# Kernel tuning notes

Hardware: AMD Instinct MI355X
Metric: run time of the kernel (lower is better)

The kernel has to match this reference:

```python
import jax, jax.numpy as jnp
import numpy as np

DIM = 1024
HEADS = 32
HEAD_DIM = DIM // HEADS
SR_RATIO = 2
N_RATIO = SR_RATIO * SR_RATIO  # AvgPool1d kernel/stride
BN_EPS = 1e-6


def setup_inputs() -> dict:
    key = jax.random.key(0)
    ks = jax.random.split(key, 10)
    B, N, C = 4, 2048, DIM
    s = C ** -0.5
    return {
        "x": jax.random.normal(ks[0], (B, N, C), dtype=jnp.float32),
        # torch.nn.Linear weights, shape [out, in]; applied as x @ W.T
        "Wq": jax.random.normal(ks[1], (C, C), dtype=jnp.float32) * s,
        "Wk": jax.random.normal(ks[2], (C, C), dtype=jnp.float32) * s,
        "Wv": jax.random.normal(ks[3], (C, C), dtype=jnp.float32) * s,
        "Wp": jax.random.normal(ks[4], (C, C), dtype=jnp.float32) * s,
        "bp": jax.random.normal(ks[5], (C,), dtype=jnp.float32) * 0.01,
        # BatchNorm1d (eval mode) affine + running stats over channel dim C
        "bn_gamma": jnp.ones((C,), dtype=jnp.float32),
        "bn_beta": jnp.zeros((C,), dtype=jnp.float32),
        "bn_mean": jax.random.normal(ks[6], (C,), dtype=jnp.float32) * 0.01,
        "bn_var": jnp.ones((C,), dtype=jnp.float32) + jax.random.uniform(ks[7], (C,), dtype=jnp.float32) * 0.1,
    }


def reference(x, Wq, Wk, Wv, Wp, bp, bn_gamma, bn_beta, bn_mean, bn_var):
    B, N, C = x.shape
    scale = HEAD_DIM ** -0.5
    # Q from full-resolution tokens
    q = (x @ Wq.T).reshape(B, N, HEADS, HEAD_DIM).transpose(0, 2, 1, 3)  # [B,H,N,d]
    # spatial reduction: AvgPool1d(kernel=N_RATIO, stride=N_RATIO) over tokens
    xr = x.reshape(B, N // N_RATIO, N_RATIO, C).mean(axis=2)  # [B,M,C]
    # BatchNorm1d eval: normalize channel dim with running stats
    xr = (xr - bn_mean) * jax.lax.rsqrt(bn_var + BN_EPS) * bn_gamma + bn_beta
    M = xr.shape[1]
    k = (xr @ Wk.T).reshape(B, M, HEADS, HEAD_DIM).transpose(0, 2, 1, 3)  # [B,H,M,d]
    v = (xr @ Wv.T).reshape(B, M, HEADS, HEAD_DIM).transpose(0, 2, 1, 3)  # [B,H,M,d]
    # NOTE: no softmax in the original module — raw scaled scores feed the second matmul
    attn = jnp.einsum("bhnd,bhmd->bhnm", q, k) * scale  # [B,H,N,M]
    out = jnp.einsum("bhnm,bhmd->bhnd", attn, v)        # [B,H,N,d]
    out = out.transpose(0, 2, 1, 3).reshape(B, N, C)
    return out @ Wp.T + bp
```

## Files before the change

### kernel.cpp

```cpp
#include <hip/hip_runtime.h>
#include <stdint.h>

#define DEVFN __device__ __forceinline__

typedef __attribute__((ext_vector_type(8))) short s16x8;
typedef __attribute__((ext_vector_type(4))) float f32x4;

DEVFN float bf2f(uint16_t u) {
  union { uint32_t i; float f; } v; v.i = ((uint32_t)u) << 16; return v.f;
}
DEVFN uint16_t f2bf(float f) {
  union { float f; uint32_t i; } v; v.f = f;
  uint32_t u = v.i;
  return (uint16_t)((u + 0x7FFFu + ((u >> 16) & 1u)) >> 16);
}

DEVFN void gload_lds16(const void* g, void* l) {
  __builtin_amdgcn_global_load_lds(
      (const __attribute__((address_space(1))) uint32_t*)g,
      (__attribute__((address_space(3))) uint32_t*)l, 16, 0, 0);
}

__global__ __launch_bounds__(256)
void prep_kernel(const float* __restrict__ x,
                 const float* __restrict__ bn_g, const float* __restrict__ bn_b,
                 const float* __restrict__ bn_m, const float* __restrict__ bn_v,
                 const float* __restrict__ Wk, const float* __restrict__ Wv,
                 const float* __restrict__ Wp,
                 uint16_t* __restrict__ Xh,
                 uint16_t* __restrict__ XRh,
                 uint16_t* __restrict__ Wkvh,
                 uint16_t* __restrict__ Wph)
{
  const int t = threadIdx.x;
  const int bid = blockIdx.x;
  if (bid < 2048) {
    const int prow = bid;
    const int c0 = t * 4;
    const size_t xbase = (size_t)prow * 4096 + c0;
    float s[4] = {0.f, 0.f, 0.f, 0.f};
#pragma unroll
    for (int r = 0; r < 4; ++r) {
      const float4 w = *(const float4*)(x + xbase + (size_t)r * 1024);
      const float vv[4] = { w.x, w.y, w.z, w.w };
      uint64_t wh = 0;
#pragma unroll
      for (int j = 0; j < 4; ++j) {
        wh |= ((uint64_t)f2bf(vv[j])) << (16 * j);
        s[j] += vv[j];
      }
      *(uint64_t*)(Xh + xbase + (size_t)r * 1024) = wh;
    }
    uint64_t wh = 0;
#pragma unroll
    for (int j = 0; j < 4; ++j) {
      const int c = c0 + j;
      const float y = (s[j] * 0.25f - bn_m[c]) / sqrtf(bn_v[c] + 1e-6f) * bn_g[c] + bn_b[c];
      wh |= ((uint64_t)f2bf(y)) << (16 * j);
    }
    *(uint64_t*)(XRh + (size_t)prow * 1024 + c0) = wh;
  } else {
    const int wb = bid - 2048;
    const int which = wb >> 10;
    const int i = (wb & 1023) * 256 + t;
    const float* src = (which == 0) ? Wk : (which == 1) ? Wv : Wp;
    const float4 v = ((const float4*)src)[i];
    const float vv[4] = { v.x, v.y, v.z, v.w };
    uint64_t wh = 0;
#pragma unroll
    for (int j = 0; j < 4; ++j)
      wh |= ((uint64_t)f2bf(vv[j])) << (16 * j);
    if (which == 2) {
      ((uint64_t*)Wph)[i] = wh;
    } else {
      ((uint64_t*)Wkvh)[(size_t)which * (1024 * 1024 / 4) + i] = wh;
    }
  }
}

template<int APARTS, int BPARTS, bool BATCHB, bool AMODA, int EPI, bool KSPLIT2,
         bool SMALLM>
__global__ __launch_bounds__(256, 2)
void gemm_nt(const uint16_t* __restrict__ A0, const uint16_t* __restrict__ A1,
             const uint16_t* __restrict__ B0, const uint16_t* __restrict__ B1,
             float* __restrict__ C32, uint16_t* __restrict__ Cb0,
             const float* __restrict__ bias,
             int M, int N, int K, int rows_per_batch)
{
  constexpr int BM = SMALLM ? 64 : 128, BN = 128, BK = 64;
  constexpr int WCN = SMALLM ? 4 : 2;
  constexpr int WNW = BN / WCN;
  constexpr int NREP = WNW / 16;
  constexpr int APASS = SMALLM ? 2 : 4;
  __shared__ uint16_t sA[APARTS][BM * BK];
  __shared__ uint16_t sB[BPARTS][BN * BK];

  const int t = threadIdx.x;
  const int lane = t & 63;
  const int wave = t >> 6;
  const int wr = wave / WCN, wc = wave % WCN;
  const int fq = lane >> 4, fr = lane & 15;

  const int nwg = gridDim.x;
  const int cpx = nwg >> 3;
  const int orig = blockIdx.x;
  const int swz = (orig & 7) * cpx + (orig >> 3);
  const int nbx = N >> 7;
  const int bm = (swz / nbx) * BM;
  const int bn = (swz % nbx) * BN;

  const uint16_t* Ap[2] = { A0, A1 };
  const uint16_t* Bp[2] = { B0, B1 };
  if (BATCHB) {
    const size_t boff = (size_t)(bm / rows_per_batch) * (size_t)N * (size_t)K;
    Bp[0] += boff;
    if (BPARTS > 1) Bp[1] += boff;
  }
  if (KSPLIT2) {
    const size_t half = (size_t)blockIdx.y * M * N;
    if (EPI == 1) Cb0 += half; else C32 += half;
  }

  f32x4 acc[4][NREP];
#pragma unroll
  for (int m = 0; m < 4; ++m)
#pragma unroll
    for (int n = 0; n < NREP; ++n) acc[m][n] = (f32x4)0.0f;

  const int nkt = K >> (KSPLIT2 ? 7 : 6);
  const int kt0 = KSPLIT2 ? (blockIdx.y * nkt) : 0;
  for (int kt = kt0; kt < kt0 + nkt; ++kt) {
    __syncthreads();
#pragma unroll
    for (int i = 0; i < APASS; ++i) {
      const int X = t * 16 + i * 4096;
      const int r = X >> 7;
      const int g = ((X >> 4) & 7) ^ (r & 7);
      const int kcol = (kt << 6) + g * 8;
      const int arow = AMODA ? ((bm + r) & 1023) : (bm + r);
      const size_t srcA = (size_t)arow * K + kcol;
#pragma unroll
      for (int p = 0; p < APARTS; ++p)
        gload_lds16(Ap[p] + srcA, (char*)(&sA[p][0]) + X);
    }
#pragma unroll
    for (int i = 0; i < 4; ++i) {
      const int X = t * 16 + i * 4096;
      const int r = X >> 7;
      const int g = ((X >> 4) & 7) ^ (r & 7);
      const int kcol = (kt << 6) + g * 8;
      const size_t srcB = (size_t)(bn + r) * K + kcol;
#pragma unroll
      for (int p = 0; p < BPARTS; ++p)
        gload_lds16(Bp[p] + srcB, (char*)(&sB[p][0]) + X);
    }
    __syncthreads();
#pragma unroll
    for (int ks = 0; ks < 2; ++ks) {
      s16x8 av[APARTS][4], bv[BPARTS][NREP];
#pragma unroll
      for (int m = 0; m < 4; ++m) {
        const int ra = wr * 64 + m * 16 + fr;
        const int offA = ra * 128 + ((((ks << 2) + fq) ^ (ra & 7)) << 4);
#pragma unroll
        for (int p = 0; p < APARTS; ++p)
          av[p][m] = *(const s16x8*)((const char*)(&sA[p][0]) + offA);
      }
#pragma unroll
      for (int n = 0; n < NREP; ++n) {
        const int rb = wc * WNW + n * 16 + fr;
        const int offB = rb * 128 + ((((ks << 2) + fq) ^ (rb & 7)) << 4);
#pragma unroll
        for (int p = 0; p < BPARTS; ++p)
          bv[p][n] = *(const s16x8*)((const char*)(&sB[p][0]) + offB);
      }
#pragma unroll
      for (int m = 0; m < 4; ++m)
#pragma unroll
        for (int n = 0; n < NREP; ++n) {
          acc[m][n] = __builtin_amdgcn_mfma_f32_16x16x32_bf16(
              av[0][m], bv[0][n], acc[m][n], 0, 0, 0);
          if constexpr (BPARTS > 1)
            acc[m][n] = __builtin_amdgcn_mfma_f32_16x16x32_bf16(
                av[0][m], bv[1][n], acc[m][n], 0, 0, 0);
          if constexpr (APARTS > 1)
            acc[m][n] = __builtin_amdgcn_mfma_f32_16x16x32_bf16(
                av[1][m], bv[0][n], acc[m][n], 0, 0, 0);
        }
    }
  }

#pragma unroll
  for (int m = 0; m < 4; ++m) {
#pragma unroll
    for (int n = 0; n < NREP; ++n) {
#pragma unroll
      for (int j = 0; j < 4; ++j) {
        const int row = bm + wr * 64 + m * 16 + fq * 4 + j;
        const int col = bn + wc * WNW + n * 16 + fr;
        const size_t idx = (size_t)row * N + col;
        float v = acc[m][n][j];
        if constexpr (EPI == 0) {
          C32[idx] = v;
        } else if constexpr (EPI == 1) {
          Cb0[idx] = f2bf(v);
        } else {
          C32[idx] = v + bias[col];
        }
      }
    }
  }
}

__global__ __launch_bounds__(256)
void kv1_kernel(const uint16_t* __restrict__ KVcat, float* __restrict__ part)
{
  const int bid = blockIdx.x;
  const int bh = bid >> 3, ch = bid & 7;
  const int b = bh >> 5, h = bh & 31;
  const int t = threadIdx.x;
  __shared__ float sK[64][32];
  __shared__ float sV[64][32];
  const int f = t >> 3, e0 = (t & 7) * 4;
  const int lr = t >> 2, q = t & 3;
  const size_t rowb = (size_t)(b * 512 + ch * 64 + lr) * 2048 + h * 32 + q * 8;
  const size_t H = (size_t)2048 * 2048;
  const s16x8 k0 = *(const s16x8*)(KVcat + rowb);
  const s16x8 k1 = *(const s16x8*)(KVcat + H + rowb);
  const s16x8 v0 = *(const s16x8*)(KVcat + rowb + 1024);
  const s16x8 v1 = *(const s16x8*)(KVcat + H + rowb + 1024);
#pragma unroll
  for (int j = 0; j < 8; ++j) {
    sK[lr][q * 8 + j] = bf2f((uint16_t)k0[j]) + bf2f((uint16_t)k1[j]);
    sV[lr][q * 8 + j] = bf2f((uint16_t)v0[j]) + bf2f((uint16_t)v1[j]);
  }
  __syncthreads();
  float a0 = 0.f, a1 = 0.f, a2 = 0.f, a3 = 0.f;
#pragma unroll 16
  for (int mm = 0; mm < 64; ++mm) {
    const float kf = sK[mm][f];
    const float4 vv = *(const float4*)&sV[mm][e0];
    a0 += kf * vv.x; a1 += kf * vv.y; a2 += kf * vv.z; a3 += kf * vv.w;
  }
  float* o = part + ((size_t)bid * 32 + f) * 32 + e0;
  o[0] = a0; o[1] = a1; o[2] = a2; o[3] = a3;
}

__global__ __launch_bounds__(256)
void t_kernel(const float* __restrict__ part, const float* __restrict__ Wq,
              uint16_t* __restrict__ Tth)
{
  const int bid = blockIdx.x;
  const int b = bid >> 7, h = (bid >> 2) & 31, cc = bid & 3;
  const int bh = b * 32 + h;
  const int t = threadIdx.x;
  __shared__ float sKV[32][32];
  {
    const int f = t >> 3, e0 = (t & 7) * 4;
    f32x4 a = (f32x4)0.0f;
#pragma unroll
    for (int ch = 0; ch < 8; ++ch)
      a += *(const f32x4*)(part + ((size_t)(bh * 8 + ch) * 32 + f) * 32 + e0);
    a *= 0.17677669529663687f;
    *(f32x4*)&sKV[f][e0] = a;
  }
  __syncthreads();
  const int c = cc * 256 + t;
  f32x4 acc[8];
#pragma unroll
  for (int i = 0; i < 8; ++i) acc[i] = (f32x4)0.0f;
  const float* wqp = Wq + (size_t)(h * 32) * 1024 + c;
#pragma unroll 8
  for (int f = 0; f < 32; ++f) {
    const float wq = wqp[(size_t)f * 1024];
#pragma unroll
    for (int i = 0; i < 8; ++i) {
      const f32x4 kv = *(const f32x4*)&sKV[f][i * 4];
      acc[i] += kv * wq;
    }
  }
  const size_t o = (((size_t)b << 10) + c) * 1024 + h * 32;
#pragma unroll
  for (int i = 0; i < 8; ++i) {
    uint64_t wh = 0;
#pragma unroll
    for (int j = 0; j < 4; ++j)
      wh |= ((uint64_t)f2bf(acc[i][j])) << (16 * j);
    *(uint64_t*)(Tth + o + i * 4) = wh;
  }
}

extern "C" void kernel_launch(void* const* d_in, const int* in_sizes, int n_in,
                              void* d_out, int out_size, void* d_ws, size_t ws_size,
                              hipStream_t stream)
{
  const float* x   = (const float*)d_in[0];
  const float* Wq  = (const float*)d_in[1];
  const float* Wk  = (const float*)d_in[2];
  const float* Wv  = (const float*)d_in[3];
  const float* Wp  = (const float*)d_in[4];
  const float* bp  = (const float*)d_in[5];
  const float* bng = (const float*)d_in[6];
  const float* bnb = (const float*)d_in[7];
  const float* bnm = (const float*)d_in[8];
  const float* bnv = (const float*)d_in[9];
  float* out = (float*)d_out;

  char* ws = (char*)d_ws;
  size_t off = 0;
  auto alloc = [&](size_t bytes) {
    char* p = ws + off;
    off += (bytes + 255) & ~(size_t)255;
    return p;
  };
  uint16_t* Xh   = (uint16_t*)alloc((size_t)8192 * 1024 * 2);
  uint16_t* XRh  = (uint16_t*)alloc((size_t)2048 * 1024 * 2);
  uint16_t* Wkvh = (uint16_t*)alloc((size_t)2048 * 1024 * 2);
  uint16_t* Wph  = (uint16_t*)alloc((size_t)1024 * 1024 * 2);
  uint16_t* KVcat= (uint16_t*)alloc((size_t)2 * 2048 * 2048 * 2);
  uint16_t* Gh   = (uint16_t*)alloc((size_t)4096 * 1024 * 2);
  uint16_t* Tth = KVcat;
  float* KVpart = (float*)Gh;

  prep_kernel<<<5120, 256, 0, stream>>>(x, bng, bnb, bnm, bnv, Wk, Wv, Wp,
                                        Xh, XRh, Wkvh, Wph);
  gemm_nt<1, 1, false, false, 1, true, false><<<dim3(256, 2), 256, 0, stream>>>(
      XRh, nullptr, Wkvh, nullptr, nullptr, KVcat, nullptr,
      2048, 2048, 1024, 1 << 30);
  kv1_kernel<<<1024, 256, 0, stream>>>(KVcat, KVpart);
  t_kernel<<<512, 256, 0, stream>>>(KVpart, Wq, Tth);
  gemm_nt<1, 1, true, true, 1, false, true><<<512, 256, 0, stream>>>(
      Wph, nullptr, Tth, nullptr, nullptr, Gh, nullptr,
      4096, 1024, 1024, 1024);
  gemm_nt<1, 1, true, false, 2, false, false><<<512, 256, 0, stream>>>(
      Xh, nullptr, Gh, nullptr, out, nullptr, bp,
      8192, 1024, 1024, 2048);
}
```

Measured before the change: 89.74 us.

## Fuse K/V projection GEMM with per-head K^T V reduction via interleaved weights

Interleaves the Wk and Wv rows per head so that a single 128-column GEMM tile holds the K and V columns of two heads. A new gemm_kv kernel computes the XR·Wkv tile with MFMA, parks it in LDS and directly reduces K^T V partials for each 64-row chunk. This removes the bf16 KVcat intermediate, the split-K write of two halves, and the separate kv1 kernel launch. In exchange the K^T V math now runs in fp32 from LDS without bf16 rounding of K and V, and there is no K split, so each block runs a longer serial K loop.

```diff
diff --git a/kernel.cpp b/kernel.cpp
--- a/kernel.cpp
+++ b/kernel.cpp
@@ -29,7 +29,7 @@
                  const float* __restrict__ Wp,
                  uint16_t* __restrict__ Xh,
                  uint16_t* __restrict__ XRh,
-                 uint16_t* __restrict__ Wkvh,
+                 uint16_t* __restrict__ Wkvi,
                  uint16_t* __restrict__ Wph)
 {
   const int t = threadIdx.x;
@@ -73,7 +73,10 @@
     if (which == 2) {
       ((uint64_t*)Wph)[i] = wh;
     } else {
-      ((uint64_t*)Wkvh)[(size_t)which * (1024 * 1024 / 4) + i] = wh;
+      const int row  = i >> 8;
+      const int col4 = i & 255;
+      const int nrow = ((row >> 5) << 6) + which * 32 + (row & 31);
+      ((uint64_t*)Wkvi)[(size_t)nrow * 256 + col4] = wh;
     }
   }
 }
@@ -212,38 +215,113 @@
   }
 }
 
-__global__ __launch_bounds__(256)
-void kv1_kernel(const uint16_t* __restrict__ KVcat, float* __restrict__ part)
+__global__ __launch_bounds__(256, 2)
+void gemm_kv(const uint16_t* __restrict__ A,
+             const uint16_t* __restrict__ B,
+             float* __restrict__ part)
 {
-  const int bid = blockIdx.x;
-  const int bh = bid >> 3, ch = bid & 7;
-  const int b = bh >> 5, h = bh & 31;
+  constexpr int BM = 64, BN = 128, BK = 64;
+  __shared__ union {
+    struct { uint16_t a[BM * BK]; uint16_t b[BN * BK]; } s;
+    float c[BM][BN];
+  } sm;
+
   const int t = threadIdx.x;
-  __shared__ float sK[64][32];
-  __shared__ float sV[64][32];
-  const int f = t >> 3, e0 = (t & 7) * 4;
-  const int lr = t >> 2, q = t & 3;
-  const size_t rowb = (size_t)(b * 512 + ch * 64 + lr) * 2048 + h * 32 + q * 8;
-  const size_t H = (size_t)2048 * 2048;
-  const s16x8 k0 = *(const s16x8*)(KVcat + rowb);
-  const s16x8 k1 = *(const s16x8*)(KVcat + H + rowb);
-  const s16x8 v0 = *(const s16x8*)(KVcat + rowb + 1024);
-  const s16x8 v1 = *(const s16x8*)(KVcat + H + rowb + 1024);
-#pragma unroll
-  for (int j = 0; j < 8; ++j) {
-    sK[lr][q * 8 + j] = bf2f((uint16_t)k0[j]) + bf2f((uint16_t)k1[j]);
-    sV[lr][q * 8 + j] = bf2f((uint16_t)v0[j]) + bf2f((uint16_t)v1[j]);
-  }
+  const int lane = t & 63;
+  const int wave = t >> 6;
+  const int wc = wave;
+  const int fq = lane >> 4, fr = lane & 15;
+
+  const int nwg = gridDim.x;
+  const int cpx = nwg >> 3;
+  const int orig = blockIdx.x;
+  const int swz = (orig & 7) * cpx + (orig >> 3);
+  const int bmI = swz >> 4;
+  const int bnI = swz & 15;
+  const int bm = bmI * BM;
+  const int bn = bnI * BN;
+
+  f32x4 acc[4][2];
+#pragma unroll
+  for (int m = 0; m < 4; ++m)
+#pragma unroll
+    for (int n = 0; n < 2; ++n) acc[m][n] = (f32x4)0.0f;
+
+  for (int kt = 0; kt < 16; ++kt) {
+    __syncthreads();
+#pragma unroll
+    for (int i = 0; i < 2; ++i) {
+      const int X = t * 16 + i * 4096;
+      const int r = X >> 7;
+      const int g = ((X >> 4) & 7) ^ (r & 7);
+      const int kcol = (kt << 6) + g * 8;
+      gload_lds16(A + (size_t)(bm + r) * 1024 + kcol, (char*)(&sm.s.a[0]) + X);
+    }
+#pragma unroll
+    for (int i = 0; i < 4; ++i) {
+      const int X = t * 16 + i * 4096;
+      const int r = X >> 7;
+      const int g = ((X >> 4) & 7) ^ (r & 7);
+      const int kcol = (kt << 6) + g * 8;
+      gload_lds16(B + (size_t)(bn + r) * 1024 + kcol, (char*)(&sm.s.b[0]) + X);
+    }
+    __syncthreads();
+#pragma unroll
+    for (int ks = 0; ks < 2; ++ks) {
+      s16x8 av[4], bv[2];
+#pragma unroll
+      for (int m = 0; m < 4; ++m) {
+        const int ra = m * 16 + fr;
+        const int offA = ra * 128 + ((((ks << 2) + fq) ^ (ra & 7)) << 4);
+        av[m] = *(const s16x8*)((const char*)(&sm.s.a[0]) + offA);
+      }
+#pragma unroll
+      for (int n = 0; n < 2; ++n) {
+        const int rb = wc * 32 + n * 16 + fr;
+        const int offB = rb * 128 + ((((ks << 2) + fq) ^ (rb & 7)) << 4);
+        bv[n] = *(const s16x8*)((const char*)(&sm.s.b[0]) + offB);
+      }
+#pragma unroll
+      for (int m = 0; m < 4; ++m)
+#pragma unroll
+        for (int n = 0; n < 2; ++n)
+          acc[m][n] = __builtin_amdgcn_mfma_f32_16x16x32_bf16(
+              av[m], bv[n], acc[m][n], 0, 0, 0);
+    }
+  }
+
   __syncthreads();
-  float a0 = 0.f, a1 = 0.f, a2 = 0.f, a3 = 0.f;
-#pragma unroll 16
-  for (int mm = 0; mm < 64; ++mm) {
-    const float kf = sK[mm][f];
-    const float4 vv = *(const float4*)&sV[mm][e0];
-    a0 += kf * vv.x; a1 += kf * vv.y; a2 += kf * vv.z; a3 += kf * vv.w;
-  }
-  float* o = part + ((size_t)bid * 32 + f) * 32 + e0;
-  o[0] = a0; o[1] = a1; o[2] = a2; o[3] = a3;
+#pragma unroll
+  for (int m = 0; m < 4; ++m)
+#pragma unroll
+    for (int n = 0; n < 2; ++n)
+#pragma unroll
+      for (int j = 0; j < 4; ++j) {
+        const int row = m * 16 + fq * 4 + j;
+        const int col = wc * 32 + n * 16 + fr;
+        sm.c[row][col] = acc[m][n][j];
+      }
+  __syncthreads();
+
+  const int hsel = t >> 7;
+  const int f  = (t >> 2) & 31;
+  const int e0 = (t & 3) * 8;
+  const int kcol = hsel * 64 + f;
+  const int vcol = hsel * 64 + 32 + e0;
+  f32x4 a0 = (f32x4)0.0f, a1 = (f32x4)0.0f;
+#pragma unroll 8
+  for (int m = 0; m < 64; ++m) {
+    const float kf = sm.c[m][kcol];
+    const f32x4 v0 = *(const f32x4*)&sm.c[m][vcol];
+    const f32x4 v1 = *(const f32x4*)&sm.c[m][vcol + 4];
+    a0 += v0 * kf;
+    a1 += v1 * kf;
+  }
+  const int b = bmI >> 3, ch = bmI & 7;
+  const int h = bnI * 2 + hsel;
+  float* o = part + (((size_t)(b * 32 + h) * 8 + ch) * 32 + f) * 32 + e0;
+  *(f32x4*)o = a0;
+  *(f32x4*)(o + 4) = a1;
 }
 
 __global__ __launch_bounds__(256)
@@ -315,19 +393,15 @@
   };
   uint16_t* Xh   = (uint16_t*)alloc((size_t)8192 * 1024 * 2);
   uint16_t* XRh  = (uint16_t*)alloc((size_t)2048 * 1024 * 2);
-  uint16_t* Wkvh = (uint16_t*)alloc((size_t)2048 * 1024 * 2);
+  uint16_t* Wkvi = (uint16_t*)alloc((size_t)2048 * 1024 * 2);
   uint16_t* Wph  = (uint16_t*)alloc((size_t)1024 * 1024 * 2);
-  uint16_t* KVcat= (uint16_t*)alloc((size_t)2 * 2048 * 2048 * 2);
+  uint16_t* Tth  = (uint16_t*)alloc((size_t)4096 * 1024 * 2);
   uint16_t* Gh   = (uint16_t*)alloc((size_t)4096 * 1024 * 2);
-  uint16_t* Tth = KVcat;
   float* KVpart = (float*)Gh;
 
   prep_kernel<<<5120, 256, 0, stream>>>(x, bng, bnb, bnm, bnv, Wk, Wv, Wp,
-                                        Xh, XRh, Wkvh, Wph);
-  gemm_nt<1, 1, false, false, 1, true, false><<<dim3(256, 2), 256, 0, stream>>>(
-      XRh, nullptr, Wkvh, nullptr, nullptr, KVcat, nullptr,
-      2048, 2048, 1024, 1 << 30);
-  kv1_kernel<<<1024, 256, 0, stream>>>(KVcat, KVpart);
+                                        Xh, XRh, Wkvi, Wph);
+  gemm_kv<<<512, 256, 0, stream>>>(XRh, Wkvi, KVpart);
   t_kernel<<<512, 256, 0, stream>>>(KVpart, Wq, Tth);
   gemm_nt<1, 1, true, true, 1, false, true><<<512, 256, 0, stream>>>(
       Wph, nullptr, Tth, nullptr, nullptr, Gh, nullptr,
```

Result: slower. 99.90 us (+11.3%).

## Double-buffer LDS tiles in gemm_nt to overlap global loads with MFMA

Applied to the files above, without the earlier changes.

Converts the GEMM main loop from single-buffered to double-buffered shared memory. The next K tile is issued via global_load_lds into the alternate buffer while the current tile is consumed, with explicit vmcnt waits and raw s_barrier in place of __syncthreads. It also drops the unused multi-part template parameters. LDS use doubles, to 64KB in the large tile case, which may limit the two-blocks-per-CU occupancy target.

```diff
diff --git a/kernel.cpp b/kernel.cpp
--- a/kernel.cpp
+++ b/kernel.cpp
@@ -78,11 +78,10 @@
   }
 }
 
-template<int APARTS, int BPARTS, bool BATCHB, bool AMODA, int EPI, bool KSPLIT2,
-         bool SMALLM>
+template<bool BATCHB, bool AMODA, int EPI, bool KSPLIT2, bool SMALLM>
 __global__ __launch_bounds__(256, 2)
-void gemm_nt(const uint16_t* __restrict__ A0, const uint16_t* __restrict__ A1,
-             const uint16_t* __restrict__ B0, const uint16_t* __restrict__ B1,
+void gemm_nt(const uint16_t* __restrict__ A0,
+             const uint16_t* __restrict__ B0,
              float* __restrict__ C32, uint16_t* __restrict__ Cb0,
              const float* __restrict__ bias,
              int M, int N, int K, int rows_per_batch)
@@ -92,8 +91,8 @@
   constexpr int WNW = BN / WCN;
   constexpr int NREP = WNW / 16;
   constexpr int APASS = SMALLM ? 2 : 4;
-  __shared__ uint16_t sA[APARTS][BM * BK];
-  __shared__ uint16_t sB[BPARTS][BN * BK];
+  __shared__ uint16_t sA[2][BM * BK];
+  __shared__ uint16_t sB[2][BN * BK];
 
   const int t = threadIdx.x;
   const int lane = t & 63;
@@ -109,13 +108,10 @@
   const int bm = (swz / nbx) * BM;
   const int bn = (swz % nbx) * BN;
 
-  const uint16_t* Ap[2] = { A0, A1 };
-  const uint16_t* Bp[2] = { B0, B1 };
-  if (BATCHB) {
-    const size_t boff = (size_t)(bm / rows_per_batch) * (size_t)N * (size_t)K;
-    Bp[0] += boff;
-    if (BPARTS > 1) Bp[1] += boff;
-  }
+  const uint16_t* Ap = A0;
+  const uint16_t* Bp = B0;
+  if (BATCHB)
+    Bp += (size_t)(bm / rows_per_batch) * (size_t)N * (size_t)K;
   if (KSPLIT2) {
     const size_t half = (size_t)blockIdx.y * M * N;
     if (EPI == 1) Cb0 += half; else C32 += half;
@@ -127,10 +123,7 @@
 #pragma unroll
     for (int n = 0; n < NREP; ++n) acc[m][n] = (f32x4)0.0f;
 
-  const int nkt = K >> (KSPLIT2 ? 7 : 6);
-  const int kt0 = KSPLIT2 ? (blockIdx.y * nkt) : 0;
-  for (int kt = kt0; kt < kt0 + nkt; ++kt) {
-    __syncthreads();
+  auto STAGE = [&](int c, int kt) {
 #pragma unroll
     for (int i = 0; i < APASS; ++i) {
       const int X = t * 16 + i * 4096;
@@ -138,10 +131,7 @@
       const int g = ((X >> 4) & 7) ^ (r & 7);
       const int kcol = (kt << 6) + g * 8;
       const int arow = AMODA ? ((bm + r) & 1023) : (bm + r);
-      const size_t srcA = (size_t)arow * K + kcol;
-#pragma unroll
-      for (int p = 0; p < APARTS; ++p)
-        gload_lds16(Ap[p] + srcA, (char*)(&sA[p][0]) + X);
+      gload_lds16(Ap + (size_t)arow * K + kcol, (char*)(&sA[c][0]) + X);
     }
 #pragma unroll
     for (int i = 0; i < 4; ++i) {
@@ -149,45 +139,54 @@
       const int r = X >> 7;
       const int g = ((X >> 4) & 7) ^ (r & 7);
       const int kcol = (kt << 6) + g * 8;
-      const size_t srcB = (size_t)(bn + r) * K + kcol;
-#pragma unroll
-      for (int p = 0; p < BPARTS; ++p)
-        gload_lds16(Bp[p] + srcB, (char*)(&sB[p][0]) + X);
-    }
-    __syncthreads();
+      gload_lds16(Bp + (size_t)(bn + r) * K + kcol, (char*)(&sB[c][0]) + X);
+    }
+  };
+
+  const int nkt = K >> (KSPLIT2 ? 7 : 6);
+  const int kt0 = KSPLIT2 ? (blockIdx.y * nkt) : 0;
+  const int ktend = kt0 + nkt;
+
+  STAGE(0, kt0);
+  int cur = 0;
+  for (int kt = kt0; kt < ktend; ++kt) {
+    __builtin_amdgcn_s_barrier();
+    if (kt + 1 < ktend) {
+      STAGE(cur ^ 1, kt + 1);
+      if constexpr (SMALLM)
+        asm volatile("s_waitcnt vmcnt(6)" ::: "memory");
+      else
+        asm volatile("s_waitcnt vmcnt(8)" ::: "memory");
+    } else {
+      asm volatile("s_waitcnt vmcnt(0)" ::: "memory");
+    }
+    __builtin_amdgcn_sched_barrier(0);
+    __builtin_amdgcn_s_barrier();
+    asm volatile("" ::: "memory");
+
 #pragma unroll
     for (int ks = 0; ks < 2; ++ks) {
-      s16x8 av[APARTS][4], bv[BPARTS][NREP];
+      s16x8 av[4], bv[NREP];
 #pragma unroll
       for (int m = 0; m < 4; ++m) {
         const int ra = wr * 64 + m * 16 + fr;
         const int offA = ra * 128 + ((((ks << 2) + fq) ^ (ra & 7)) << 4);
-#pragma unroll
-        for (int p = 0; p < APARTS; ++p)
-          av[p][m] = *(const s16x8*)((const char*)(&sA[p][0]) + offA);
+        av[m] = *(const s16x8*)((const char*)(&sA[cur][0]) + offA);
       }
 #pragma unroll
       for (int n = 0; n < NREP; ++n) {
         const int rb = wc * WNW + n * 16 + fr;
         const int offB = rb * 128 + ((((ks << 2) + fq) ^ (rb & 7)) << 4);
-#pragma unroll
-        for (int p = 0; p < BPARTS; ++p)
-          bv[p][n] = *(const s16x8*)((const char*)(&sB[p][0]) + offB);
+        bv[n] = *(const s16x8*)((const char*)(&sB[cur][0]) + offB);
       }
 #pragma unroll
       for (int m = 0; m < 4; ++m)
 #pragma unroll
-        for (int n = 0; n < NREP; ++n) {
+        for (int n = 0; n < NREP; ++n)
           acc[m][n] = __builtin_amdgcn_mfma_f32_16x16x32_bf16(
-              av[0][m], bv[0][n], acc[m][n], 0, 0, 0);
-          if constexpr (BPARTS > 1)
-            acc[m][n] = __builtin_amdgcn_mfma_f32_16x16x32_bf16(
-                av[0][m], bv[1][n], acc[m][n], 0, 0, 0);
-          if constexpr (APARTS > 1)
-            acc[m][n] = __builtin_amdgcn_mfma_f32_16x16x32_bf16(
-                av[1][m], bv[0][n], acc[m][n], 0, 0, 0);
-        }
-    }
+              av[m], bv[n], acc[m][n], 0, 0, 0);
+    }
+    cur ^= 1;
   }
 
 #pragma unroll
@@ -324,15 +323,15 @@
 
   prep_kernel<<<5120, 256, 0, stream>>>(x, bng, bnb, bnm, bnv, Wk, Wv, Wp,
                                         Xh, XRh, Wkvh, Wph);
-  gemm_nt<1, 1, false, false, 1, true, false><<<dim3(256, 2), 256, 0, stream>>>(
-      XRh, nullptr, Wkvh, nullptr, nullptr, KVcat, nullptr,
+  gemm_nt<false, false, 1, true, false><<<dim3(256, 2), 256, 0, stream>>>(
+      XRh, Wkvh, nullptr, KVcat, nullptr,
       2048, 2048, 1024, 1 << 30);
   kv1_kernel<<<1024, 256, 0, stream>>>(KVcat, KVpart);
   t_kernel<<<512, 256, 0, stream>>>(KVpart, Wq, Tth);
-  gemm_nt<1, 1, true, true, 1, false, true><<<512, 256, 0, stream>>>(
-      Wph, nullptr, Tth, nullptr, nullptr, Gh, nullptr,
+  gemm_nt<true, true, 1, false, true><<<512, 256, 0, stream>>>(
+      Wph, Tth, nullptr, Gh, nullptr,
       4096, 1024, 1024, 1024);
-  gemm_nt<1, 1, true, false, 2, false, false><<<512, 256, 0, stream>>>(
-      Xh, nullptr, Gh, nullptr, out, nullptr, bp,
+  gemm_nt<true, false, 2, false, false><<<512, 256, 0, stream>>>(
+      Xh, Gh, out, nullptr, bp,
       8192, 1024, 1024, 2048);
 }
```

New measurement: 89.49 us. Within noise of the previous version (-0.3%).
